# Kernel tuning notes

Measured on AMD Instinct MI355X. Metric: run time of the kernel, lower is better.

The kernel has to match this reference:

```python
import jax, jax.numpy as jnp
import numpy as np

N_NODES = 100000
N_EDGES = 800000
IN = 128
HID = 128
EMB = 64
OUT = 8
N_GRAPHS = 64


def setup_inputs() -> dict:
    key = jax.random.key(0)
    ks = jax.random.split(key, 12)
    x = jax.random.normal(ks[0], (N_NODES, IN), dtype=jnp.float32)
    edge_index = jax.random.randint(ks[1], (2, N_EDGES), 0, N_NODES, dtype=jnp.int64)
    batch = jnp.sort(jax.random.randint(ks[2], (N_NODES,), 0, N_GRAPHS, dtype=jnp.int64))
    embed = jax.random.normal(ks[3], (N_GRAPHS, EMB), dtype=jnp.float32)
    s_in = 1.0 / np.sqrt(IN).astype(np.float32)
    s_h = 1.0 / np.sqrt(HID).astype(np.float32)
    s_l = 1.0 / np.sqrt(HID + EMB).astype(np.float32)
    return {
        "x": x,
        "edge_index": edge_index,
        "batch": batch,
        "embed": embed,
        # SAGEConv1: out = lin_l(mean_agg) + lin_r(x); bias lives in lin_l
        "W1l": jax.random.normal(ks[4], (HID, IN), dtype=jnp.float32) * s_in,
        "b1l": jnp.zeros((HID,), dtype=jnp.float32),
        "W1r": jax.random.normal(ks[5], (HID, IN), dtype=jnp.float32) * s_in,
        # SAGEConv2
        "W2l": jax.random.normal(ks[6], (HID, HID), dtype=jnp.float32) * s_h,
        "b2l": jnp.zeros((HID,), dtype=jnp.float32),
        "W2r": jax.random.normal(ks[7], (HID, HID), dtype=jnp.float32) * s_h,
        # final Linear(hidden + embed_dim, out)
        "Wlin": jax.random.normal(ks[8], (OUT, HID + EMB), dtype=jnp.float32) * s_l,
        "blin": jnp.zeros((OUT,), dtype=jnp.float32),
    }


def _segment_mean(vals, idx, num_segments):
    # scatter-mean with count clamped to 1 (matches PyG scatter 'mean')
    s = jax.ops.segment_sum(vals, idx, num_segments=num_segments)
    c = jax.ops.segment_sum(jnp.ones((vals.shape[0], 1), vals.dtype), idx,
                            num_segments=num_segments)
    return s / jnp.maximum(c, 1.0)


def reference(x, edge_index, batch, embed, W1l, b1l, W1r, W2l, b2l, W2r, Wlin, blin):
    src, dst = edge_index[0], edge_index[1]

    def sage(h, Wl, bl, Wr):
        # gather source features, mean-aggregate at destination, then linear
        agg = _segment_mean(h[src], dst, N_NODES)          # [N, d]
        return agg @ Wl.T + bl + h @ Wr.T                   # [N, HID]

    h = jax.nn.relu(sage(x, W1l, b1l, W1r))
    h = jax.nn.relu(sage(h, W2l, b2l, W2r))
    pooled = _segment_mean(h, batch, N_GRAPHS)              # [G, HID]
    z = jnp.concatenate([pooled, embed], axis=1)            # [G, HID+EMB]
    return z @ Wlin.T + blin                                # [G, OUT]
```

## Files before the change

### kernel.cpp

```cpp
#include <hip/hip_runtime.h>
#include <stdint.h>

#define FEAT   128
#define GR     64
#define LDA    136
#define NBUCK  256
#define BSHIFT 9

typedef __attribute__((ext_vector_type(8))) short bf8_t;
typedef __attribute__((ext_vector_type(4))) float f4_t;

__device__ inline float bf2f(ushort h){
    union { uint u; float f; } v; v.u = ((uint)h) << 16; return v.f;
}
__device__ inline float bf2f_lo(uint u){
    union { uint u; float f; } v; v.u = u << 16; return v.f;
}
__device__ inline float bf2f_hi(uint u){
    union { uint u; float f; } v; v.u = u & 0xffff0000u; return v.f;
}
__device__ inline ushort f2bf(float f){
    union { float f; uint u; } v; v.f = f;
    uint r = (v.u + 0x7FFFu + ((v.u >> 16) & 1u)) >> 16;
    return (ushort)r;
}

__global__ __launch_bounds__(256) void k_prep(
    const float* __restrict__ x, ushort* __restrict__ xb, int n4, int nbCast,
    const float* __restrict__ a0, const float* __restrict__ a1,
    const float* __restrict__ a2, const float* __restrict__ a3,
    ushort* __restrict__ o0, ushort* __restrict__ o1,
    ushort* __restrict__ o2, ushort* __restrict__ o3,
    const int* __restrict__ dst, int* __restrict__ bcnt, int E)
{
    int bid = blockIdx.x;
    if (bid < nbCast){
        int i = bid * 256 + threadIdx.x;
        if (i >= n4) return;
        float4 v = ((const float4*)x)[i];
        ushort4 o; o.x = f2bf(v.x); o.y = f2bf(v.y); o.z = f2bf(v.z); o.w = f2bf(v.w);
        ((ushort4*)xb)[i] = o;
        return;
    }
    if (bid < nbCast + 64){
        int i = (bid - nbCast) * 256 + threadIdx.x;
        int sel = i >> 12, j = i & 4095;
        const float* s = sel == 0 ? a0 : sel == 1 ? a1 : sel == 2 ? a2 : a3;
        ushort*      d = sel == 0 ? o0 : sel == 1 ? o1 : sel == 2 ? o2 : o3;
        float4 v = ((const float4*)s)[j];
        ushort4 o; o.x = f2bf(v.x); o.y = f2bf(v.y); o.z = f2bf(v.z); o.w = f2bf(v.w);
        ((ushort4*)d)[j] = o;
        return;
    }
    __shared__ int h[NBUCK];
    h[threadIdx.x] = 0;
    __syncthreads();
    int base = (bid - nbCast - 64) * 4096 + threadIdx.x;
    #pragma unroll
    for (int k = 0; k < 16; k++){
        int e = base + k * 256;
        if (e < E) atomicAdd(&h[dst[e] >> BSHIFT], 1);
    }
    __syncthreads();
    int c = h[threadIdx.x];
    if (c) atomicAdd(&bcnt[threadIdx.x], c);
}

__global__ void k_bscan(const int* __restrict__ bcnt, int* __restrict__ bbase,
                        int* __restrict__ bpos, int* __restrict__ rowp,
                        int* __restrict__ csr, float* __restrict__ pooled,
                        int E, int M){
    __shared__ int sd[NBUCK];
    int t = threadIdx.x;
    #pragma unroll
    for (int k = 0; k < 32; k++) pooled[t * 32 + k] = 0.f;
    int v = bcnt[t];
    sd[t] = v; __syncthreads();
    for (int off = 1; off < NBUCK; off <<= 1){
        int x = (t >= off) ? sd[t - off] : 0;
        __syncthreads();
        sd[t] += x;
        __syncthreads();
    }
    int ex = sd[t] - v;
    bbase[t] = ex;
    bpos[t]  = ex;
    if (t < 8) csr[E + t] = 0;
    if (t == NBUCK - 1){ bbase[NBUCK] = sd[t]; rowp[M] = E; }
}

__global__ __launch_bounds__(256) void k_bucket(const int* __restrict__ src,
                                                const int* __restrict__ dst,
                                                int* __restrict__ bpos,
                                                int2* __restrict__ bp, int E){
    __shared__ int h[NBUCK];
    __shared__ int bb[NBUCK];
    int t = threadIdx.x;
    h[t] = 0;
    __syncthreads();
    int base = blockIdx.x * 4096 + t;
    int bk[16], sv[16], dv[16];
    #pragma unroll
    for (int k = 0; k < 16; k++){
        int e = base + k * 256;
        if (e < E){
            dv[k] = dst[e]; sv[k] = src[e];
            bk[k] = dv[k] >> BSHIFT;
            atomicAdd(&h[bk[k]], 1);
        } else bk[k] = -1;
    }
    __syncthreads();
    int c = h[t];
    bb[t] = c ? atomicAdd(&bpos[t], c) : 0;
    __syncthreads();
    h[t] = 0;
    __syncthreads();
    #pragma unroll
    for (int k = 0; k < 16; k++){
        if (bk[k] >= 0){
            int r = atomicAdd(&h[bk[k]], 1);
            bp[bb[bk[k]] + r] = make_int2(sv[k], dv[k]);
        }
    }
}

__global__ __launch_bounds__(512) void k_csr(const int2* __restrict__ bp,
                                             const int* __restrict__ bbase,
                                             int* __restrict__ rowp,
                                             int* __restrict__ csr, int M){
    __shared__ int cnt[512];
    __shared__ int sd[512];
    int b = blockIdx.x, t = threadIdx.x;
    int nbase = b << BSHIFT;
    int nnodes = min(512, M - nbase);
    int e0 = bbase[b], e1 = bbase[b + 1];
    cnt[t] = 0;
    __syncthreads();
    for (int e = e0 + t; e < e1; e += 512)
        atomicAdd(&cnt[bp[e].y - nbase], 1);
    __syncthreads();
    int v = cnt[t];
    sd[t] = v; __syncthreads();
    for (int off = 1; off < 512; off <<= 1){
        int x = (t >= off) ? sd[t - off] : 0;
        __syncthreads();
        sd[t] += x;
        __syncthreads();
    }
    int ex = sd[t] - v;
    if (t < nnodes) rowp[nbase + t] = e0 + ex;
    cnt[t] = ex;
    __syncthreads();
    for (int e = e0 + t; e < e1; e += 512){
        int2 pr = bp[e];
        int r = atomicAdd(&cnt[pr.y - nbase], 1);
        csr[e0 + r] = pr.x;
    }
}

#define ACCA(vv)                                   \
    a0 += bf2f_lo((vv).x); a1 += bf2f_hi((vv).x);  \
    a2 += bf2f_lo((vv).y); a3 += bf2f_hi((vv).y);  \
    a4 += bf2f_lo((vv).z); a5 += bf2f_hi((vv).z);  \
    a6 += bf2f_lo((vv).w); a7 += bf2f_hi((vv).w);
#define ACCB(vv)                                   \
    b0 += bf2f_lo((vv).x); b1 += bf2f_hi((vv).x);  \
    b2 += bf2f_lo((vv).y); b3 += bf2f_hi((vv).y);  \
    b4 += bf2f_lo((vv).z); b5 += bf2f_hi((vv).z);  \
    b6 += bf2f_lo((vv).w); b7 += bf2f_hi((vv).w);

__global__ __launch_bounds__(256) void k_agg(const ushort* __restrict__ srcf,
                                             const int* __restrict__ rowp,
                                             const int* __restrict__ csr,
                                             ushort* __restrict__ aggb, int M){
    int node = blockIdx.x * 16 + (threadIdx.x >> 4);
    int l    = threadIdx.x & 15;
    if (node >= M) return;
    int s = rowp[node], e = rowp[node + 1];
    const char* base = (const char*)srcf + (uint)l * 16u;
    float a0 = 0.f, a1 = 0.f, a2 = 0.f, a3 = 0.f;
    float a4 = 0.f, a5 = 0.f, a6 = 0.f, a7 = 0.f;
    float b0 = 0.f, b1 = 0.f, b2 = 0.f, b3 = 0.f;
    float b4 = 0.f, b5 = 0.f, b6 = 0.f, b7 = 0.f;
    int i = s;
    for (; i + 8 <= e; i += 8){
        int idx[8];
        __builtin_memcpy(idx, csr + i, 32);
        uint4 v0 = *(const uint4*)(base + ((uint)idx[0] << 8));
        uint4 v1 = *(const uint4*)(base + ((uint)idx[1] << 8));
        uint4 v2 = *(const uint4*)(base + ((uint)idx[2] << 8));
        uint4 v3 = *(const uint4*)(base + ((uint)idx[3] << 8));
        uint4 v4 = *(const uint4*)(base + ((uint)idx[4] << 8));
        uint4 v5 = *(const uint4*)(base + ((uint)idx[5] << 8));
        uint4 v6 = *(const uint4*)(base + ((uint)idx[6] << 8));
        uint4 v7 = *(const uint4*)(base + ((uint)idx[7] << 8));
        ACCA(v0); ACCA(v1); ACCA(v2); ACCA(v3);
        ACCB(v4); ACCB(v5); ACCB(v6); ACCB(v7);
    }
    if (i + 4 <= e){
        int idx[4];
        __builtin_memcpy(idx, csr + i, 16);
        uint4 v0 = *(const uint4*)(base + ((uint)idx[0] << 8));
        uint4 v1 = *(const uint4*)(base + ((uint)idx[1] << 8));
        uint4 v2 = *(const uint4*)(base + ((uint)idx[2] << 8));
        uint4 v3 = *(const uint4*)(base + ((uint)idx[3] << 8));
        ACCA(v0); ACCA(v1); ACCB(v2); ACCB(v3);
        i += 4;
    }
    for (; i < e; i++){
        uint4 v = *(const uint4*)(base + ((uint)csr[i] << 8));
        ACCA(v);
    }
    float inv = (e > s) ? 1.0f / (float)(e - s) : 0.f;
    uint4 o;
    o.x = ((uint)f2bf((a1 + b1) * inv) << 16) | (uint)f2bf((a0 + b0) * inv);
    o.y = ((uint)f2bf((a3 + b3) * inv) << 16) | (uint)f2bf((a2 + b2) * inv);
    o.z = ((uint)f2bf((a5 + b5) * inv) << 16) | (uint)f2bf((a4 + b4) * inv);
    o.w = ((uint)f2bf((a7 + b7) * inv) << 16) | (uint)f2bf((a6 + b6) * inv);
    *(uint4*)(aggb + (size_t)node * FEAT + l * 8) = o;
}

__global__ __launch_bounds__(512) void k_gemm(
    const ushort* __restrict__ Aagg, const ushort* __restrict__ Aself,
    const ushort* __restrict__ Wl, const ushort* __restrict__ Wr,
    const float* __restrict__ bias, ushort* __restrict__ Hout, int M, int mode,
    float* __restrict__ pooled, const int* __restrict__ batch)
{
    __shared__ ushort Bs[128 * LDA];
    const int tid  = threadIdx.x;
    const int lane = tid & 63;
    const int wave = tid >> 6;
    const int l15  = lane & 15;
    const int quad = lane >> 4;
    const int m0   = blockIdx.x * 128;

    int arow = m0 + wave * 16 + l15;
    if (arow >= M) arow = M - 1;
    const ushort* ap0 = Aagg  + (size_t)arow * FEAT + quad * 8;
    const ushort* ap1 = Aself + (size_t)arow * FEAT + quad * 8;

    f4_t acc[8];
    #pragma unroll
    for (int i = 0; i < 8; i++) acc[i] = (f4_t){0.f, 0.f, 0.f, 0.f};

    #pragma unroll
    for (int pass = 0; pass < 2; pass++){
        const ushort* Ap = pass ? ap1 : ap0;
        const ushort* Wp = pass ? Wr  : Wl;
        #pragma unroll
        for (int it = 0; it < 4; it++){
            int idx = (it * 512 + tid) * 8;
            int r = idx >> 7, c = idx & 127;
            *(int4*)(&Bs[r * LDA + c]) = *(const int4*)(Wp + idx);
        }
        bf8_t ga0 = *(const bf8_t*)(Ap);
        bf8_t ga1 = *(const bf8_t*)(Ap + 32);
        bf8_t ga2 = *(const bf8_t*)(Ap + 64);
        bf8_t ga3 = *(const bf8_t*)(Ap + 96);
        __syncthreads();
        const ushort* brow = &Bs[l15 * LDA + quad * 8];
        #pragma unroll
        for (int nt = 0; nt < 8; nt++){
            const ushort* b = brow + nt * 16 * LDA;
            acc[nt] = __builtin_amdgcn_mfma_f32_16x16x32_bf16(ga0, *(const bf8_t*)(b),      acc[nt], 0, 0, 0);
            acc[nt] = __builtin_amdgcn_mfma_f32_16x16x32_bf16(ga1, *(const bf8_t*)(b + 32), acc[nt], 0, 0, 0);
            acc[nt] = __builtin_amdgcn_mfma_f32_16x16x32_bf16(ga2, *(const bf8_t*)(b + 64), acc[nt], 0, 0, 0);
            acc[nt] = __builtin_amdgcn_mfma_f32_16x16x32_bf16(ga3, *(const bf8_t*)(b + 96), acc[nt], 0, 0, 0);
        }
        __syncthreads();
    }

    if (mode == 0){
        #pragma unroll
        for (int nt = 0; nt < 8; nt++){
            int col = nt * 16 + l15;
            float bcol = bias[col];
            #pragma unroll
            for (int reg = 0; reg < 4; reg++){
                int gm = m0 + wave * 16 + quad * 4 + reg;
                if (gm < M){
                    float v = acc[nt][reg] + bcol;
                    v = v > 0.f ? v : 0.f;
                    Hout[(size_t)gm * FEAT + col] = f2bf(v);
                }
            }
        }
        return;
    }

    float* ps = (float*)Bs;
    int gfirst = batch[m0];
    int glast  = batch[min(m0 + 127, M - 1)];
    if (m0 + 128 <= M && gfirst == glast){
        #pragma unroll
        for (int nt = 0; nt < 8; nt++){
            float bcol = bias[nt * 16 + l15];
            float v = 0.f;
            #pragma unroll
            for (int reg = 0; reg < 4; reg++){
                float t = acc[nt][reg] + bcol;
                v += t > 0.f ? t : 0.f;
            }
            v += __shfl_xor(v, 16);
            v += __shfl_xor(v, 32);
            if (lane < 16) ps[wave * FEAT + nt * 16 + l15] = v;
        }
        __syncthreads();
        if (tid < FEAT){
            float s = 0.f;
            #pragma unroll
            for (int w8 = 0; w8 < 8; w8++) s += ps[w8 * FEAT + tid];
            atomicAdd(&pooled[gfirst * FEAT + tid], s);
        }
        return;
    }
    {
        int row0 = m0 + wave * 16 + quad * 4;
        bool wfull = (m0 + wave * 16 + 16 <= M);
        if (wfull){
            int4 gq = *(const int4*)(batch + row0);
            int g_lo = __shfl(gq.x, 0);
            int g_hi = __shfl(gq.w, 48);
            if (g_lo == g_hi){
                #pragma unroll
                for (int nt = 0; nt < 8; nt++){
                    float bcol = bias[nt * 16 + l15];
                    float v = 0.f;
                    #pragma unroll
                    for (int reg = 0; reg < 4; reg++){
                        float t = acc[nt][reg] + bcol;
                        v += t > 0.f ? t : 0.f;
                    }
                    v += __shfl_xor(v, 16);
                    v += __shfl_xor(v, 32);
                    if (lane < 16)
                        atomicAdd(&pooled[g_lo * FEAT + nt * 16 + l15], v);
                }
            } else {
                #pragma unroll
                for (int nt = 0; nt < 8; nt++){
                    int col = nt * 16 + l15;
                    float bcol = bias[col];
                    float s = 0.f; int g = gq.x;
                    #pragma unroll
                    for (int reg = 0; reg < 4; reg++){
                        int gn = reg == 0 ? gq.x : reg == 1 ? gq.y : reg == 2 ? gq.z : gq.w;
                        float t = acc[nt][reg] + bcol;
                        t = t > 0.f ? t : 0.f;
                        if (gn != g){ atomicAdd(&pooled[g * FEAT + col], s); s = 0.f; g = gn; }
                        s += t;
                    }
                    atomicAdd(&pooled[g * FEAT + col], s);
                }
            }
        } else if (row0 < M){
            #pragma unroll
            for (int nt = 0; nt < 8; nt++){
                int col = nt * 16 + l15;
                float bcol = bias[col];
                #pragma unroll
                for (int reg = 0; reg < 4; reg++){
                    int gm = row0 + reg;
                    if (gm < M){
                        float t = acc[nt][reg] + bcol;
                        t = t > 0.f ? t : 0.f;
                        atomicAdd(&pooled[batch[gm] * FEAT + col], t);
                    }
                }
            }
        }
    }
}

__global__ void k_final(const float* __restrict__ pooled, const int* __restrict__ batch,
                        const float* __restrict__ embed, const float* __restrict__ Wlin,
                        const float* __restrict__ blin, float* __restrict__ out, int M){
    int t = threadIdx.x;
    if (t >= GR * 8) return;
    int g = t >> 3, o = t & 7;
    int lo = 0, hi = M;
    while (lo < hi){ int mid = (lo + hi) >> 1; if (batch[mid] < g) lo = mid + 1; else hi = mid; }
    int s0 = lo;
    lo = s0; hi = M;
    while (lo < hi){ int mid = (lo + hi) >> 1; if (batch[mid] < g + 1) lo = mid + 1; else hi = mid; }
    int c = lo - s0;
    float inv = (c > 0) ? 1.0f / (float)c : 0.f;
    float acc = blin[o];
    const float* wr = Wlin + o * (FEAT + GR);
    for (int k = 0; k < FEAT; k++) acc += pooled[g * FEAT + k] * inv * wr[k];
    for (int k = 0; k < GR; k++)   acc += embed[g * GR + k] * wr[FEAT + k];
    out[g * 8 + o] = acc;
}

extern "C" void kernel_launch(void* const* d_in, const int* in_sizes, int n_in,
                              void* d_out, int out_size, void* d_ws, size_t ws_size,
                              hipStream_t stream)
{
    const float* x     = (const float*)d_in[0];
    const int*   eidx  = (const int*)d_in[1];
    const int*   batch = (const int*)d_in[2];
    const float* embed = (const float*)d_in[3];
    const float* W1l   = (const float*)d_in[4];
    const float* b1l   = (const float*)d_in[5];
    const float* W1r   = (const float*)d_in[6];
    const float* W2l   = (const float*)d_in[7];
    const float* b2l   = (const float*)d_in[8];
    const float* W2r   = (const float*)d_in[9];
    const float* Wlin  = (const float*)d_in[10];
    const float* blin  = (const float*)d_in[11];
    float* out = (float*)d_out;

    const int M = in_sizes[0] / FEAT;
    const int E = in_sizes[1] / 2;
    const int* src = eidx;
    const int* dst = eidx + E;

    char* w = (char*)d_ws;
    size_t off = 0;
    auto alloc = [&](size_t sz){ void* p = w + off; off = (off + sz + 255) & ~(size_t)255; return p; };
    ushort* xb     = (ushort*)alloc((size_t)M * FEAT * 2);
    ushort* aggb   = (ushort*)alloc((size_t)M * FEAT * 2);
    ushort* h1b    = (ushort*)alloc((size_t)M * FEAT * 2);
    int*    rowp   = (int*)alloc((size_t)(M + 1) * 4);
    int*    csr    = (int*)alloc((size_t)(E + 8) * 4);
    int*    bcnt   = (int*)alloc(NBUCK * 4);
    int*    bbase  = (int*)alloc((NBUCK + 1) * 4);
    int*    bpos   = (int*)alloc(NBUCK * 4);
    float*  pooled = (float*)alloc((size_t)GR * FEAT * 4);
    ushort* w1lb   = (ushort*)alloc((size_t)FEAT * FEAT * 2);
    ushort* w1rb   = (ushort*)alloc((size_t)FEAT * FEAT * 2);
    ushort* w2lb   = (ushort*)alloc((size_t)FEAT * FEAT * 2);
    ushort* w2rb   = (ushort*)alloc((size_t)FEAT * FEAT * 2);
    int2*   bp     = (int2*)aggb;

    hipMemsetAsync(bcnt, 0, NBUCK * 4, stream);

    const int n4     = M * FEAT / 4;
    const int nbCast = (n4 + 255) / 256;
    const int nb     = (M + 511) >> BSHIFT;
    const int ebk    = (E + 4095) / 4096;
    const int gemmb  = (M + 127) / 128;
    k_prep  <<<nbCast + 64 + ebk, 256, 0, stream>>>(x, xb, n4, nbCast,
                                                    W1l, W1r, W2l, W2r,
                                                    w1lb, w1rb, w2lb, w2rb,
                                                    dst, bcnt, E);
    k_bscan <<<1, NBUCK, 0, stream>>>(bcnt, bbase, bpos, rowp, csr, pooled, E, M);
    k_bucket<<<ebk, 256, 0, stream>>>(src, dst, bpos, bp, E);
    k_csr   <<<nb, 512, 0, stream>>>(bp, bbase, rowp, csr, M);
    k_agg   <<<(M + 15) / 16, 256, 0, stream>>>(xb, rowp, csr, aggb, M);
    k_gemm  <<<gemmb, 512, 0, stream>>>(aggb, xb, w1lb, w1rb, b1l, h1b, M, 0,
                                        nullptr, nullptr);
    k_agg   <<<(M + 15) / 16, 256, 0, stream>>>(h1b, rowp, csr, aggb, M);
    k_gemm  <<<gemmb, 512, 0, stream>>>(aggb, h1b, w2lb, w2rb, b2l, nullptr, M, 1,
                                        pooled, batch);
    k_final <<<1, 512, 0, stream>>>(pooled, batch, embed, Wlin, blin, out, M);
}
```

Measured before the change: 284.1 us.

## Build CSR via per-node degree atomics and direct fill instead of bucket sort

Replaces the two-pass bucket sort (bucket scatter into a pair buffer, then per-bucket local CSR build) with a per-node degree histogram computed during prep. Row pointers come from a blocked scan of degrees plus the bucket bases, and a fill kernel places each edge using an atomic decrement of its node's degree. This removes the intermediate pair buffer traffic and one pass over the edges. In exchange it adds global atomics on random node addresses and a larger memset, and the neighbour order within each row becomes nondeterministic.

```diff
diff --git a/kernel.cpp b/kernel.cpp
--- a/kernel.cpp
+++ b/kernel.cpp
@@ -31,7 +31,8 @@
     const float* __restrict__ a2, const float* __restrict__ a3,
     ushort* __restrict__ o0, ushort* __restrict__ o1,
     ushort* __restrict__ o2, ushort* __restrict__ o3,
-    const int* __restrict__ dst, int* __restrict__ bcnt, int E)
+    const int* __restrict__ dst, int* __restrict__ bcnt,
+    int* __restrict__ deg, int E)
 {
     int bid = blockIdx.x;
     if (bid < nbCast){
@@ -59,7 +60,11 @@
     #pragma unroll
     for (int k = 0; k < 16; k++){
         int e = base + k * 256;
-        if (e < E) atomicAdd(&h[dst[e] >> BSHIFT], 1);
+        if (e < E){
+            int d = dst[e];
+            atomicAdd(&h[d >> BSHIFT], 1);
+            atomicAdd(&deg[d], 1);
+        }
     }
     __syncthreads();
     int c = h[threadIdx.x];
@@ -67,9 +72,8 @@
 }
 
 __global__ void k_bscan(const int* __restrict__ bcnt, int* __restrict__ bbase,
-                        int* __restrict__ bpos, int* __restrict__ rowp,
-                        int* __restrict__ csr, float* __restrict__ pooled,
-                        int E, int M){
+                        int* __restrict__ rowp, int* __restrict__ csr,
+                        float* __restrict__ pooled, int E, int M){
     __shared__ int sd[NBUCK];
     int t = threadIdx.x;
     #pragma unroll
@@ -82,64 +86,19 @@
         sd[t] += x;
         __syncthreads();
     }
-    int ex = sd[t] - v;
-    bbase[t] = ex;
-    bpos[t]  = ex;
+    bbase[t] = sd[t] - v;
     if (t < 8) csr[E + t] = 0;
     if (t == NBUCK - 1){ bbase[NBUCK] = sd[t]; rowp[M] = E; }
 }
 
-__global__ __launch_bounds__(256) void k_bucket(const int* __restrict__ src,
-                                                const int* __restrict__ dst,
-                                                int* __restrict__ bpos,
-                                                int2* __restrict__ bp, int E){
-    __shared__ int h[NBUCK];
-    __shared__ int bb[NBUCK];
-    int t = threadIdx.x;
-    h[t] = 0;
-    __syncthreads();
-    int base = blockIdx.x * 4096 + t;
-    int bk[16], sv[16], dv[16];
-    #pragma unroll
-    for (int k = 0; k < 16; k++){
-        int e = base + k * 256;
-        if (e < E){
-            dv[k] = dst[e]; sv[k] = src[e];
-            bk[k] = dv[k] >> BSHIFT;
-            atomicAdd(&h[bk[k]], 1);
-        } else bk[k] = -1;
-    }
-    __syncthreads();
-    int c = h[t];
-    bb[t] = c ? atomicAdd(&bpos[t], c) : 0;
-    __syncthreads();
-    h[t] = 0;
-    __syncthreads();
-    #pragma unroll
-    for (int k = 0; k < 16; k++){
-        if (bk[k] >= 0){
-            int r = atomicAdd(&h[bk[k]], 1);
-            bp[bb[bk[k]] + r] = make_int2(sv[k], dv[k]);
-        }
-    }
-}
-
-__global__ __launch_bounds__(512) void k_csr(const int2* __restrict__ bp,
-                                             const int* __restrict__ bbase,
-                                             int* __restrict__ rowp,
-                                             int* __restrict__ csr, int M){
-    __shared__ int cnt[512];
+__global__ __launch_bounds__(512) void k_rowp(const int* __restrict__ deg,
+                                              const int* __restrict__ bbase,
+                                              int* __restrict__ rowp, int M){
     __shared__ int sd[512];
     int b = blockIdx.x, t = threadIdx.x;
     int nbase = b << BSHIFT;
     int nnodes = min(512, M - nbase);
-    int e0 = bbase[b], e1 = bbase[b + 1];
-    cnt[t] = 0;
-    __syncthreads();
-    for (int e = e0 + t; e < e1; e += 512)
-        atomicAdd(&cnt[bp[e].y - nbase], 1);
-    __syncthreads();
-    int v = cnt[t];
+    int v = (t < nnodes) ? deg[nbase + t] : 0;
     sd[t] = v; __syncthreads();
     for (int off = 1; off < 512; off <<= 1){
         int x = (t >= off) ? sd[t - off] : 0;
@@ -147,14 +106,33 @@
         sd[t] += x;
         __syncthreads();
     }
-    int ex = sd[t] - v;
-    if (t < nnodes) rowp[nbase + t] = e0 + ex;
-    cnt[t] = ex;
-    __syncthreads();
-    for (int e = e0 + t; e < e1; e += 512){
-        int2 pr = bp[e];
-        int r = atomicAdd(&cnt[pr.y - nbase], 1);
-        csr[e0 + r] = pr.x;
+    if (t < nnodes) rowp[nbase + t] = bbase[b] + sd[t] - v;
+}
+
+__global__ __launch_bounds__(256) void k_fill(const int* __restrict__ src,
+                                              const int* __restrict__ dst,
+                                              const int* __restrict__ rowp,
+                                              int* __restrict__ deg,
+                                              int* __restrict__ csr, int E){
+    int i4 = blockIdx.x * 256 + threadIdx.x;
+    int e = i4 * 4;
+    if (e + 4 <= E){
+        int4 s = ((const int4*)src)[i4];
+        int4 d = ((const int4*)dst)[i4];
+        int p0 = rowp[d.x] + atomicSub(&deg[d.x], 1) - 1; csr[p0] = s.x;
+        int p1 = rowp[d.y] + atomicSub(&deg[d.y], 1) - 1; csr[p1] = s.y;
+        int p2 = rowp[d.z] + atomicSub(&deg[d.z], 1) - 1; csr[p2] = s.z;
+        int p3 = rowp[d.w] + atomicSub(&deg[d.w], 1) - 1; csr[p3] = s.w;
+    } else {
+        #pragma unroll
+        for (int k = 0; k < 4; k++){
+            int ee = e + k;
+            if (ee < E){
+                int d = dst[ee];
+                int p = rowp[d] + atomicSub(&deg[d], 1) - 1;
+                csr[p] = src[ee];
+            }
+        }
     }
 }
 
@@ -424,29 +402,29 @@
     int*    rowp   = (int*)alloc((size_t)(M + 1) * 4);
     int*    csr    = (int*)alloc((size_t)(E + 8) * 4);
     int*    bcnt   = (int*)alloc(NBUCK * 4);
+    int*    deg    = (int*)alloc((size_t)M * 4);
     int*    bbase  = (int*)alloc((NBUCK + 1) * 4);
-    int*    bpos   = (int*)alloc(NBUCK * 4);
     float*  pooled = (float*)alloc((size_t)GR * FEAT * 4);
     ushort* w1lb   = (ushort*)alloc((size_t)FEAT * FEAT * 2);
     ushort* w1rb   = (ushort*)alloc((size_t)FEAT * FEAT * 2);
     ushort* w2lb   = (ushort*)alloc((size_t)FEAT * FEAT * 2);
     ushort* w2rb   = (ushort*)alloc((size_t)FEAT * FEAT * 2);
-    int2*   bp     = (int2*)aggb;
-
-    hipMemsetAsync(bcnt, 0, NBUCK * 4, stream);
+
+    hipMemsetAsync(bcnt, 0, NBUCK * 4 + (size_t)M * 4, stream);
 
     const int n4     = M * FEAT / 4;
     const int nbCast = (n4 + 255) / 256;
     const int nb     = (M + 511) >> BSHIFT;
     const int ebk    = (E + 4095) / 4096;
     const int gemmb  = (M + 127) / 128;
+    const int fillb  = (E / 4 + 255) / 256;
     k_prep  <<<nbCast + 64 + ebk, 256, 0, stream>>>(x, xb, n4, nbCast,
                                                     W1l, W1r, W2l, W2r,
                                                     w1lb, w1rb, w2lb, w2rb,
-                                                    dst, bcnt, E);
-    k_bscan <<<1, NBUCK, 0, stream>>>(bcnt, bbase, bpos, rowp, csr, pooled, E, M);
-    k_bucket<<<ebk, 256, 0, stream>>>(src, dst, bpos, bp, E);
-    k_csr   <<<nb, 512, 0, stream>>>(bp, bbase, rowp, csr, M);
+                                                    dst, bcnt, deg, E);
+    k_bscan <<<1, NBUCK, 0, stream>>>(bcnt, bbase, rowp, csr, pooled, E, M);
+    k_rowp  <<<nb, 512, 0, stream>>>(deg, bbase, rowp, M);
+    k_fill  <<<fillb, 256, 0, stream>>>(src, dst, rowp, deg, csr, E);
     k_agg   <<<(M + 15) / 16, 256, 0, stream>>>(xb, rowp, csr, aggb, M);
     k_gemm  <<<gemmb, 512, 0, stream>>>(aggb, xb, w1lb, w1rb, b1l, h1b, M, 0,
                                         nullptr, nullptr);
```

Result: slower. 347.5 us (+22.3%).
